# Kernel tuning notes

Hardware: AMD Instinct MI355X
Metric: run time of the kernel (lower is better)

## Reference

```python
import jax, jax.numpy as jnp
import numpy as np

NUM_HEADS = 16
ROPE_THETA = 10000.0


def _vision_rope_tables(seq_len, head_dim):
    # Llama4 vision ('mllama4') 2D rotary: x/y patch-grid positions,
    # interleaved (non-neox) complex pairs. Returns cos/sin [S, head_dim//2].
    idx = int(np.sqrt(seq_len))  # patches per side (24 for 336/14)
    pos = np.arange(seq_len)
    fx = (pos % idx + 1).astype(np.float32)
    fy = (pos // idx + 1).astype(np.float32)
    freq_dim = head_dim // 2
    rope_freq = 1.0 / ROPE_THETA ** (
        np.arange(0, freq_dim, 2)[: freq_dim // 2].astype(np.float32) / freq_dim
    )
    fx = np.repeat(fx[:, None] * rope_freq[None, :], 2, axis=-1)  # [S, freq_dim]
    fy = np.repeat(fy[:, None] * rope_freq[None, :], 2, axis=-1)
    freqs = np.concatenate([fx, fy], axis=-1)[:, ::2]  # [S, head_dim//2]
    return jnp.asarray(np.cos(freqs)), jnp.asarray(np.sin(freqs))


def _apply_rope(x, cos, sin):
    # x: [B, S, H, D]; even/odd interleaved pairs treated as complex numbers
    B, S, H, D = x.shape
    xr = x.reshape(B, S, H, D // 2, 2)
    x0, x1 = xr[..., 0], xr[..., 1]
    c = cos[None, :, None, :]
    s = sin[None, :, None, :]
    o0 = x0 * c - x1 * s
    o1 = x0 * s + x1 * c
    return jnp.stack([o0, o1], axis=-1).reshape(B, S, H, D)


def setup_inputs() -> dict:
    key = jax.random.key(0)
    ks = jax.random.split(key, 5)
    E = 1408
    B, S = 16, 576
    scale = 0.02
    return {
        "hidden_states": jax.random.normal(ks[0], (B, S, E), dtype=jnp.float32),
        "w_qkv": jax.random.normal(ks[1], (E, 3 * E), dtype=jnp.float32) * scale,
        "b_qkv": jax.random.normal(ks[2], (3 * E,), dtype=jnp.float32) * scale,
        "w_o": jax.random.normal(ks[3], (E, E), dtype=jnp.float32) * scale,
        "b_o": jax.random.normal(ks[4], (E,), dtype=jnp.float32) * scale,
    }


def reference(hidden_states, w_qkv, b_qkv, w_o, b_o):
    B, S, E = hidden_states.shape
    H = NUM_HEADS
    D = E // H
    scaling = D ** -0.5

    qkv = hidden_states @ w_qkv + b_qkv  # [B,S,3E]
    q, k, v = jnp.split(qkv, 3, axis=-1)
    q = q.reshape(B, S, H, D)
    k = k.reshape(B, S, H, D)
    v = v.reshape(B, S, H, D)

    cos, sin = _vision_rope_tables(S, D)
    q = _apply_rope(q, cos, sin)
    k = _apply_rope(k, cos, sin)

    q = q * scaling
    scores = jnp.einsum("bqhd,bkhd->bhqk", q, k)  # full bidirectional attention
    probs = jax.nn.softmax(scores, axis=-1)
    attn = jnp.einsum("bhqk,bkhd->bqhd", probs, v).reshape(B, S, E)

    return attn @ w_o + b_o
```

## Files before the change

kernel.cpp:

```cpp
#include <hip/hip_runtime.h>
#include <hip/hip_bf16.h>


typedef unsigned short UST;
typedef __attribute__((ext_vector_type(8))) __bf16 bf16x8;
typedef __attribute__((ext_vector_type(4))) float f32x4;
typedef __attribute__((ext_vector_type(8))) UST us8;
typedef __attribute__((ext_vector_type(4))) UST us4;

typedef __attribute__((address_space(3))) unsigned int lds_u32;
typedef const __attribute__((address_space(1))) unsigned int glob_u32;

static __device__ __forceinline__ UST f2bf(float f){
  unsigned int x = __builtin_bit_cast(unsigned int, f);
  x += 0x7fffu + ((x >> 16) & 1u);
  return (UST)(x >> 16);
}

__global__ void k_prep(float* __restrict__ cs2,
                       UST* __restrict__ qa, UST* __restrict__ ka, UST* __restrict__ vt){
  const int x = blockIdx.x;
  const int t = threadIdx.x;
  if (t < 44){
    int p = t;
    int tt = p % 22;
    double comp = (p < 22) ? (double)(x % 24 + 1) : (double)(x / 24 + 1);
    double a = comp * pow(10000.0, -(double)tt / 22.0);
    cs2[x*88 + 2*p]     = (float)cos(a);
    cs2[x*88 + 2*p + 1] = (float)sin(a);
  }
  int c = x*256 + t;
  int bh = c / 576, s = c - bh*576;
  us8 z = {0,0,0,0,0,0,0,0};
  *(us8*)(qa + ((size_t)bh*576 + s)*96 + 88) = z;
  *(us8*)(ka + ((size_t)bh*576 + s)*96 + 88) = z;
  *(us8*)(vt + (size_t)bh*55296 + 50688 + s*8) = z;
}

__global__ void k_cvt(const float* __restrict__ in, UST* __restrict__ out, int n4){
  int i = blockIdx.x * 256 + threadIdx.x;
  if (i >= n4) return;
  float4 v = ((const float4*)in)[i];
  us4 o; o[0]=f2bf(v.x); o[1]=f2bf(v.y); o[2]=f2bf(v.z); o[3]=f2bf(v.w);
  *(us4*)(out + 4*(size_t)i) = o;
}

__global__ void k_cvt_t(const float* __restrict__ W, UST* __restrict__ Bt, int K, int N){
  __shared__ __align__(16) UST tl[64][70];
  int kt = blockIdx.x, nt = blockIdx.y;
  int t = threadIdx.x;
  int k = t >> 2, u = t & 3;
  const float* src = W + (size_t)(kt*64 + k)*N + nt*64 + u*16;
#pragma unroll
  for (int i = 0; i < 4; ++i){
    float4 v = *(const float4*)(src + 4*i);
    UST* d = &tl[k][u*16 + 4*i];
    d[0]=f2bf(v.x); d[1]=f2bf(v.y); d[2]=f2bf(v.z); d[3]=f2bf(v.w);
  }
  __syncthreads();
  int n = t >> 2;
  UST* dst = Bt + (size_t)(nt*64 + n)*K + kt*64 + u*16;
#pragma unroll
  for (int i = 0; i < 2; ++i){
    us8 o;
#pragma unroll
    for (int j = 0; j < 8; ++j) o[j] = tl[u*16 + 8*i + j][n];
    *(us8*)(dst + 8*i) = o;
  }
}

template<int EPI>
__global__ __launch_bounds__(256, 2) void k_gemm(
    const UST* __restrict__ A, const UST* __restrict__ Bt,
    const float* __restrict__ bias, void* __restrict__ Cout,
    int M, int N, int K,
    UST* __restrict__ qa, UST* __restrict__ ka, UST* __restrict__ vt,
    const float* __restrict__ cs2)
{
  __shared__ __align__(16) char SMEM[65536];
  UST (*lA)[128][64] = reinterpret_cast<UST(*)[128][64]>(SMEM);
  UST (*lB)[128][64] = reinterpret_cast<UST(*)[128][64]>(SMEM + 32768);
  float* sm = reinterpret_cast<float*>(SMEM);

  const int t = threadIdx.x;
  const int bm = blockIdx.x, bn = blockIdx.y;
  const int wave = t >> 6, lane = t & 63;
  const int lm = lane & 15, g = lane >> 4;
  const int wr = (wave >> 1) << 6, wc = (wave & 1) << 6;
  const int lrow = lane >> 3;
  const int lcol = (((lane & 7) ^ lrow) << 3);
  const UST* Ag = A  + (size_t)(bm*128 + wave*32 + lrow)*K + lcol;
  const UST* Bg = Bt + (size_t)(bn*128 + wave*32 + lrow)*K + lcol;

  f32x4 zero = {0.f,0.f,0.f,0.f};
  f32x4 acc[4][4];
#pragma unroll
  for (int i=0;i<4;++i)
#pragma unroll
    for (int j=0;j<4;++j) acc[i][j] = zero;

  const int nkt = K >> 6;
  auto stage = [&](int kt, int buf){
#pragma unroll
    for (int c = 0; c < 4; ++c){
      __builtin_amdgcn_global_load_lds((glob_u32*)(Ag + (size_t)kt*64 + (size_t)(8*c)*K),
                                       (lds_u32*)(&lA[buf][wave*32 + 8*c][0]), 16, 0, 0);
      __builtin_amdgcn_global_load_lds((glob_u32*)(Bg + (size_t)kt*64 + (size_t)(8*c)*K),
                                       (lds_u32*)(&lB[buf][wave*32 + 8*c][0]), 16, 0, 0);
    }
  };

  stage(0, 0);
  __syncthreads();
  const int swz = (lm & 7) << 3;

  for (int kt = 0; kt < nkt; ++kt){
    const int cur = kt & 1;
    if (kt + 1 < nkt) stage(kt + 1, cur ^ 1);
#pragma unroll
    for (int ks = 0; ks < 2; ++ks){
      bf16x8 af[4], bfv[4];
      const int cb = (ks*32 + g*8) ^ swz;
#pragma unroll
      for (int mf = 0; mf < 4; ++mf)
        af[mf] = __builtin_bit_cast(bf16x8, *(const us8*)&lA[cur][wr + mf*16 + lm][cb]);
#pragma unroll
      for (int nf = 0; nf < 4; ++nf)
        bfv[nf] = __builtin_bit_cast(bf16x8, *(const us8*)&lB[cur][wc + nf*16 + lm][cb]);
#pragma unroll
      for (int mf = 0; mf < 4; ++mf)
#pragma unroll
        for (int nf = 0; nf < 4; ++nf)
          acc[mf][nf] = __builtin_amdgcn_mfma_f32_16x16x32_bf16(af[mf], bfv[nf], acc[mf][nf], 0, 0, 0);
    }
    __syncthreads();
  }

  if (EPI == 0){
#pragma unroll
    for (int nf = 0; nf < 4; ++nf){
      const int col = bn*128 + wc + nf*16 + lm;
      const float bv = bias[col];
#pragma unroll
      for (int mf = 0; mf < 4; ++mf){
        const size_t rb = (size_t)(bm*128 + wr + mf*16 + g*4);
#pragma unroll
        for (int r = 0; r < 4; ++r)
          ((float*)Cout)[(rb + r)*(size_t)N + col] = acc[mf][nf][r] + bv;
      }
    }
  } else {
#pragma unroll
    for (int nf = 0; nf < 4; ++nf){
      const int col = wc + nf*16 + lm;
      const float bv = bias[bn*128 + col];
#pragma unroll
      for (int mf = 0; mf < 4; ++mf){
#pragma unroll
        for (int r = 0; r < 4; ++r){
          const int row = wr + mf*16 + g*4 + r;
          const int colS = (((col >> 3) ^ (row & 15)) << 3) | (col & 7);
          sm[row*128 + colS] = acc[mf][nf][r] + bv;
        }
      }
    }
    __syncthreads();

    const int j = bn / 11;
    const int bnr = bn - j*11;
    if (j == 2){
#pragma unroll
      for (int i = 0; i < 8; ++i){
        const int idx = t + 256*i;
        const int col = idx & 127, rch = idx >> 7;
        const int cv = bnr*128 + col;
        const int h = cv / 88, dv = cv - h*88;
        const int s0g = bm*128 + rch*8;
        const int b2 = s0g / 576, sl = s0g - b2*576;
        us8 o;
#pragma unroll
        for (int k = 0; k < 8; ++k){
          const int row = rch*8 + k;
          const int colS = (((col >> 3) ^ (row & 15)) << 3) | (col & 7);
          o[k] = f2bf(sm[row*128 + colS]);
        }
        *(us8*)(vt + ((size_t)(b2*16 + h)*96 + dv)*576 + sl) = o;
      }
    } else {
      UST* outp = j ? ka : qa;
      const float sc = j ? 1.0f : 0.10660035817780521f;
#pragma unroll
      for (int i = 0; i < 8; ++i){
        const int idx = t + 256*i;
        const int ch = idx & 15, rr = idx >> 4;
        const int cv = bnr*128 + ch*8;
        const int h = cv / 88, d0 = cv - h*88;
        const int rb = bm*128 + rr;
        const int b2 = rb / 576, s = rb - b2*576;
        const float* src = &sm[rr*128 + ((ch ^ (rr & 15)) << 3)];
        float x[8];
#pragma unroll
        for (int k = 0; k < 8; ++k) x[k] = src[k];
        const float* tb = cs2 + s*88 + d0;
        float4 q0 = *(const float4*)(tb);
        float4 q1 = *(const float4*)(tb + 4);
        float cc[4]  = {q0.x, q0.z, q1.x, q1.z};
        float ssv[4] = {q0.y, q0.w, q1.y, q1.w};
        us8 o;
#pragma unroll
        for (int p = 0; p < 4; ++p){
          float o0 = (x[2*p]*cc[p]  - x[2*p+1]*ssv[p]) * sc;
          float o1 = (x[2*p]*ssv[p] + x[2*p+1]*cc[p])  * sc;
          o[2*p] = f2bf(o0); o[2*p+1] = f2bf(o1);
        }
        *(us8*)(outp + ((size_t)(b2*16 + h)*576 + s)*96 + d0) = o;
      }
    }
  }
}

__global__ __launch_bounds__(256, 2) void k_attn(
    const UST* __restrict__ qa, const UST* __restrict__ ka,
    const UST* __restrict__ vt, UST* __restrict__ outp)
{
  __shared__ __align__(16) UST lK[64][104];
  __shared__ __align__(16) UST lV[96][72];
  __shared__ __align__(16) UST lP[4][16][72];
  const int bh = blockIdx.x, qt = blockIdx.y;
  const int t = threadIdx.x, wave = t >> 6, lane = t & 63;
  const int lm = lane & 15, g = lane >> 4;
  const int h = bh & 15, b = bh >> 4;

  bf16x8 qf[3];
  {
    const UST* qp = qa + ((size_t)bh*576 + qt*64 + wave*16 + lm)*96 + g*8;
#pragma unroll
    for (int ks = 0; ks < 3; ++ks) qf[ks] = __builtin_bit_cast(bf16x8, *(const us8*)(qp + ks*32));
  }
  f32x4 zero = {0.f,0.f,0.f,0.f};
  f32x4 acc[6];
#pragma unroll
  for (int i = 0; i < 6; ++i) acc[i] = zero;
  float psum[4];
#pragma unroll
  for (int r = 0; r < 4; ++r) psum[r] = 0.f;

  const UST* kbase = ka + (size_t)bh*576*96;
  const UST* vbase = vt + (size_t)bh*96*576;

  for (int kvt = 0; kvt < 9; ++kvt){
    {
      int r = t >> 2, u = t & 3;
      const UST* src = kbase + (size_t)(kvt*64 + r)*96 + u*24;
#pragma unroll
      for (int i = 0; i < 3; ++i)
        *(uint4*)&lK[r][u*24 + i*8] = *(const uint4*)(src + i*8);
    }
    if (t < 192){
      int d = t >> 1, hf = t & 1;
      const UST* src = vbase + (size_t)d*576 + kvt*64 + hf*32;
#pragma unroll
      for (int i = 0; i < 4; ++i)
        *(uint4*)&lV[d][hf*32 + i*8] = *(const uint4*)(src + i*8);
    }
    __syncthreads();

    f32x4 sc[4];
#pragma unroll
    for (int i = 0; i < 4; ++i) sc[i] = zero;
    __builtin_amdgcn_s_setprio(1);
#pragma unroll
    for (int ks = 0; ks < 3; ++ks){
#pragma unroll
      for (int nf = 0; nf < 4; ++nf){
        bf16x8 kf = __builtin_bit_cast(bf16x8, *(const us8*)&lK[nf*16 + lm][ks*32 + g*8]);
        sc[nf] = __builtin_amdgcn_mfma_f32_16x16x32_bf16(qf[ks], kf, sc[nf], 0, 0, 0);
      }
    }
    __builtin_amdgcn_s_setprio(0);

#pragma unroll
    for (int r = 0; r < 4; ++r){
      float ls = 0.f;
#pragma unroll
      for (int nf = 0; nf < 4; ++nf){
        float p = __expf(sc[nf][r]);
        sc[nf][r] = p;
        ls += p;
      }
      psum[r] += ls;
    }

#pragma unroll
    for (int nf = 0; nf < 4; ++nf)
#pragma unroll
      for (int r = 0; r < 4; ++r)
        lP[wave][4*g + r][nf*16 + lm] = f2bf(sc[nf][r]);

    bf16x8 pa[2];
#pragma unroll
    for (int ks2 = 0; ks2 < 2; ++ks2)
      pa[ks2] = __builtin_bit_cast(bf16x8, *(const us8*)&lP[wave][lm][ks2*32 + g*8]);
    __builtin_amdgcn_s_setprio(1);
#pragma unroll
    for (int ks2 = 0; ks2 < 2; ++ks2)
#pragma unroll
      for (int df = 0; df < 6; ++df){
        bf16x8 vf = __builtin_bit_cast(bf16x8, *(const us8*)&lV[df*16 + lm][ks2*32 + g*8]);
        acc[df] = __builtin_amdgcn_mfma_f32_16x16x32_bf16(pa[ks2], vf, acc[df], 0, 0, 0);
      }
    __builtin_amdgcn_s_setprio(0);
    __syncthreads();
  }

#pragma unroll
  for (int m = 1; m <= 8; m <<= 1)
#pragma unroll
    for (int r = 0; r < 4; ++r) psum[r] += __shfl_xor(psum[r], m, 64);
  float inv[4];
#pragma unroll
  for (int r = 0; r < 4; ++r) inv[r] = 1.f / psum[r];

  const size_t rowt = (size_t)b*576 + qt*64 + wave*16;
#pragma unroll
  for (int df = 0; df < 6; ++df){
    int d = df*16 + lm;
    if (d < 88){
#pragma unroll
      for (int r = 0; r < 4; ++r)
        outp[(rowt + 4*g + r)*1408 + h*88 + d] = f2bf(acc[df][r] * inv[r]);
    }
  }
}

extern "C" void kernel_launch(void* const* d_in, const int* in_sizes, int n_in,
                              void* d_out, int out_size, void* d_ws, size_t ws_size,
                              hipStream_t stream)
{
  (void)in_sizes; (void)n_in; (void)out_size; (void)ws_size;
  const float* hs   = (const float*)d_in[0];
  const float* wqkv = (const float*)d_in[1];
  const float* bqkv = (const float*)d_in[2];
  const float* wo   = (const float*)d_in[3];
  const float* bo   = (const float*)d_in[4];
  float* out = (float*)d_out;

  char* w = (char*)d_ws;
  UST* A_bf   = (UST*)(w);
  UST* Bt1    = (UST*)(w + 25952256);
  UST* Bt2    = (UST*)(w + 37847040);
  UST* qa     = (UST*)(w + 41811968);
  UST* ka     = (UST*)(w + 70123520);
  UST* vt     = (UST*)(w + 98435072);
  float* cs2  = (float*)(w + 126746624);

  k_prep<<<576, 256, 0, stream>>>(cs2, qa, ka, vt);
  k_cvt<<<12672, 256, 0, stream>>>(hs, A_bf, 3244032);
  k_cvt_t<<<dim3(22, 66), 256, 0, stream>>>(wqkv, Bt1, 1408, 4224);
  k_cvt_t<<<dim3(22, 22), 256, 0, stream>>>(wo, Bt2, 1408, 1408);
  k_gemm<3><<<dim3(72, 33), 256, 0, stream>>>(A_bf, Bt1, bqkv, nullptr, 9216, 4224, 1408,
                                              qa, ka, vt, cs2);
  k_attn<<<dim3(256, 9), 256, 0, stream>>>(qa, ka, vt, A_bf);
  k_gemm<0><<<dim3(72, 11), 256, 0, stream>>>(A_bf, Bt2, bo, out, 9216, 1408, 1408,
                                              nullptr, nullptr, nullptr, nullptr);
}
```

Before: 291.2 us.

## Merge prep/convert launches, change epilogue swizzle, widen attention KV tiles

```diff
diff --git a/kernel.cpp b/kernel.cpp
--- a/kernel.cpp
+++ b/kernel.cpp
@@ -17,40 +17,45 @@
   return (UST)(x >> 16);
 }
 
-__global__ void k_prep(float* __restrict__ cs2,
-                       UST* __restrict__ qa, UST* __restrict__ ka, UST* __restrict__ vt){
-  const int x = blockIdx.x;
-  const int t = threadIdx.x;
-  if (t < 44){
-    int p = t;
-    int tt = p % 22;
-    double comp = (p < 22) ? (double)(x % 24 + 1) : (double)(x / 24 + 1);
-    double a = comp * pow(10000.0, -(double)tt / 22.0);
-    cs2[x*88 + 2*p]     = (float)cos(a);
-    cs2[x*88 + 2*p + 1] = (float)sin(a);
-  }
-  int c = x*256 + t;
-  int bh = c / 576, s = c - bh*576;
-  us8 z = {0,0,0,0,0,0,0,0};
-  *(us8*)(qa + ((size_t)bh*576 + s)*96 + 88) = z;
-  *(us8*)(ka + ((size_t)bh*576 + s)*96 + 88) = z;
-  *(us8*)(vt + (size_t)bh*55296 + 50688 + s*8) = z;
-}
-
-__global__ void k_cvt(const float* __restrict__ in, UST* __restrict__ out, int n4){
+__global__ void k_cvt(const float* __restrict__ in, UST* __restrict__ out, int n4,
+                      float* __restrict__ cs2,
+                      UST* __restrict__ qa, UST* __restrict__ ka, UST* __restrict__ vt){
   int i = blockIdx.x * 256 + threadIdx.x;
-  if (i >= n4) return;
-  float4 v = ((const float4*)in)[i];
-  us4 o; o[0]=f2bf(v.x); o[1]=f2bf(v.y); o[2]=f2bf(v.z); o[3]=f2bf(v.w);
-  *(us4*)(out + 4*(size_t)i) = o;
-}
-
-__global__ void k_cvt_t(const float* __restrict__ W, UST* __restrict__ Bt, int K, int N){
+  if (i < n4){
+    float4 v = ((const float4*)in)[i];
+    us4 o; o[0]=f2bf(v.x); o[1]=f2bf(v.y); o[2]=f2bf(v.z); o[3]=f2bf(v.w);
+    *(us4*)(out + 4*(size_t)i) = o;
+  }
+  if (blockIdx.x < 576){
+    const int x = blockIdx.x, t = threadIdx.x;
+    if (t < 44){
+      int p = t;
+      int tt = p % 22;
+      double comp = (p < 22) ? (double)(x % 24 + 1) : (double)(x / 24 + 1);
+      double a = comp * pow(10000.0, -(double)tt / 22.0);
+      cs2[x*88 + 2*p]     = (float)cos(a);
+      cs2[x*88 + 2*p + 1] = (float)sin(a);
+    }
+    int c = x*256 + t;
+    int bh = c / 576, s = c - bh*576;
+    us8 z = {0,0,0,0,0,0,0,0};
+    *(us8*)(qa + ((size_t)bh*576 + s)*96 + 88) = z;
+    *(us8*)(ka + ((size_t)bh*576 + s)*96 + 88) = z;
+    *(us8*)(vt + (size_t)bh*55296 + 50688 + s*8) = z;
+  }
+}
+
+__global__ void k_cvt_t(const float* __restrict__ Wq, const float* __restrict__ Wo,
+                        UST* __restrict__ Bt1, UST* __restrict__ Bt2){
   __shared__ __align__(16) UST tl[64][70];
+  const int K = 1408;
   int kt = blockIdx.x, nt = blockIdx.y;
+  const float* W; UST* Bt; int N, ntl;
+  if (nt < 66){ W = Wq; Bt = Bt1; N = 4224; ntl = nt; }
+  else        { W = Wo; Bt = Bt2; N = 1408; ntl = nt - 66; }
   int t = threadIdx.x;
   int k = t >> 2, u = t & 3;
-  const float* src = W + (size_t)(kt*64 + k)*N + nt*64 + u*16;
+  const float* src = W + (size_t)(kt*64 + k)*N + ntl*64 + u*16;
 #pragma unroll
   for (int i = 0; i < 4; ++i){
     float4 v = *(const float4*)(src + 4*i);
@@ -59,7 +64,7 @@
   }
   __syncthreads();
   int n = t >> 2;
-  UST* dst = Bt + (size_t)(nt*64 + n)*K + kt*64 + u*16;
+  UST* dst = Bt + (size_t)(ntl*64 + n)*K + kt*64 + u*16;
 #pragma unroll
   for (int i = 0; i < 2; ++i){
     us8 o;
@@ -159,7 +164,8 @@
 #pragma unroll
         for (int r = 0; r < 4; ++r){
           const int row = wr + mf*16 + g*4 + r;
-          const int colS = (((col >> 3) ^ (row & 15)) << 3) | (col & 7);
+          const int sw2 = (row ^ (row >> 2)) & 3;
+          const int colS = (((col >> 3) ^ sw2) << 3) | (col & 7);
           sm[row*128 + colS] = acc[mf][nf][r] + bv;
         }
       }
@@ -181,7 +187,8 @@
 #pragma unroll
         for (int k = 0; k < 8; ++k){
           const int row = rch*8 + k;
-          const int colS = (((col >> 3) ^ (row & 15)) << 3) | (col & 7);
+          const int sw2 = (row ^ (row >> 2)) & 3;
+          const int colS = (((col >> 3) ^ sw2) << 3) | (col & 7);
           o[k] = f2bf(sm[row*128 + colS]);
         }
         *(us8*)(vt + ((size_t)(b2*16 + h)*96 + dv)*576 + sl) = o;
@@ -197,7 +204,8 @@
         const int h = cv / 88, d0 = cv - h*88;
         const int rb = bm*128 + rr;
         const int b2 = rb / 576, s = rb - b2*576;
-        const float* src = &sm[rr*128 + ((ch ^ (rr & 15)) << 3)];
+        const int sw2 = (rr ^ (rr >> 2)) & 3;
+        const float* src = &sm[rr*128 + ((ch ^ sw2) << 3)];
         float x[8];
 #pragma unroll
         for (int k = 0; k < 8; ++k) x[k] = src[k];
@@ -223,9 +231,9 @@
     const UST* __restrict__ qa, const UST* __restrict__ ka,
     const UST* __restrict__ vt, UST* __restrict__ outp)
 {
-  __shared__ __align__(16) UST lK[64][104];
-  __shared__ __align__(16) UST lV[96][72];
-  __shared__ __align__(16) UST lP[4][16][72];
+  __shared__ __align__(16) UST lK[96][104];
+  __shared__ __align__(16) UST lV[96][104];
+  __shared__ __align__(16) UST lP[4][16][104];
   const int bh = blockIdx.x, qt = blockIdx.y;
   const int t = threadIdx.x, wave = t >> 6, lane = t & 63;
   const int lm = lane & 15, g = lane >> 4;
@@ -248,31 +256,27 @@
   const UST* kbase = ka + (size_t)bh*576*96;
   const UST* vbase = vt + (size_t)bh*96*576;
 
-  for (int kvt = 0; kvt < 9; ++kvt){
-    {
-      int r = t >> 2, u = t & 3;
-      const UST* src = kbase + (size_t)(kvt*64 + r)*96 + u*24;
-#pragma unroll
-      for (int i = 0; i < 3; ++i)
-        *(uint4*)&lK[r][u*24 + i*8] = *(const uint4*)(src + i*8);
-    }
+  for (int kvt = 0; kvt < 6; ++kvt){
     if (t < 192){
-      int d = t >> 1, hf = t & 1;
-      const UST* src = vbase + (size_t)d*576 + kvt*64 + hf*32;
-#pragma unroll
-      for (int i = 0; i < 4; ++i)
-        *(uint4*)&lV[d][hf*32 + i*8] = *(const uint4*)(src + i*8);
+      const int r = t >> 1, half = t & 1;
+      const UST* srcK = kbase + (size_t)(kvt*96 + r)*96 + half*48;
+      const UST* srcV = vbase + (size_t)r*576 + kvt*96 + half*48;
+#pragma unroll
+      for (int i2 = 0; i2 < 6; ++i2){
+        *(uint4*)&lK[r][half*48 + i2*8] = *(const uint4*)(srcK + i2*8);
+        *(uint4*)&lV[r][half*48 + i2*8] = *(const uint4*)(srcV + i2*8);
+      }
     }
     __syncthreads();
 
-    f32x4 sc[4];
-#pragma unroll
-    for (int i = 0; i < 4; ++i) sc[i] = zero;
+    f32x4 sc[6];
+#pragma unroll
+    for (int i = 0; i < 6; ++i) sc[i] = zero;
     __builtin_amdgcn_s_setprio(1);
 #pragma unroll
     for (int ks = 0; ks < 3; ++ks){
 #pragma unroll
-      for (int nf = 0; nf < 4; ++nf){
+      for (int nf = 0; nf < 6; ++nf){
         bf16x8 kf = __builtin_bit_cast(bf16x8, *(const us8*)&lK[nf*16 + lm][ks*32 + g*8]);
         sc[nf] = __builtin_amdgcn_mfma_f32_16x16x32_bf16(qf[ks], kf, sc[nf], 0, 0, 0);
       }
@@ -283,7 +287,7 @@
     for (int r = 0; r < 4; ++r){
       float ls = 0.f;
 #pragma unroll
-      for (int nf = 0; nf < 4; ++nf){
+      for (int nf = 0; nf < 6; ++nf){
         float p = __expf(sc[nf][r]);
         sc[nf][r] = p;
         ls += p;
@@ -292,18 +296,18 @@
     }
 
 #pragma unroll
-    for (int nf = 0; nf < 4; ++nf)
+    for (int nf = 0; nf < 6; ++nf)
 #pragma unroll
       for (int r = 0; r < 4; ++r)
         lP[wave][4*g + r][nf*16 + lm] = f2bf(sc[nf][r]);
 
-    bf16x8 pa[2];
-#pragma unroll
-    for (int ks2 = 0; ks2 < 2; ++ks2)
+    bf16x8 pa[3];
+#pragma unroll
+    for (int ks2 = 0; ks2 < 3; ++ks2)
       pa[ks2] = __builtin_bit_cast(bf16x8, *(const us8*)&lP[wave][lm][ks2*32 + g*8]);
     __builtin_amdgcn_s_setprio(1);
 #pragma unroll
-    for (int ks2 = 0; ks2 < 2; ++ks2)
+    for (int ks2 = 0; ks2 < 3; ++ks2)
 #pragma unroll
       for (int df = 0; df < 6; ++df){
         bf16x8 vf = __builtin_bit_cast(bf16x8, *(const us8*)&lV[df*16 + lm][ks2*32 + g*8]);
@@ -354,10 +358,8 @@
   UST* vt     = (UST*)(w + 98435072);
   float* cs2  = (float*)(w + 126746624);
 
-  k_prep<<<576, 256, 0, stream>>>(cs2, qa, ka, vt);
-  k_cvt<<<12672, 256, 0, stream>>>(hs, A_bf, 3244032);
-  k_cvt_t<<<dim3(22, 66), 256, 0, stream>>>(wqkv, Bt1, 1408, 4224);
-  k_cvt_t<<<dim3(22, 22), 256, 0, stream>>>(wo, Bt2, 1408, 1408);
+  k_cvt<<<12672, 256, 0, stream>>>(hs, A_bf, 3244032, cs2, qa, ka, vt);
+  k_cvt_t<<<dim3(22, 88), 256, 0, stream>>>(wqkv, wo, Bt1, Bt2);
   k_gemm<3><<<dim3(72, 33), 256, 0, stream>>>(A_bf, Bt1, bqkv, nullptr, 9216, 4224, 1408,
                                               qa, ka, vt, cs2);
   k_attn<<<dim3(256, 9), 256, 0, stream>>>(qa, ka, vt, A_bf);
```

New measurement: 284.0 us (median of 2 runs). 1.03x faster.
